# Optimization experiments

Hardware: AMD Instinct MI355X
Metric: run time of the kernel (lower is better)

## Reference

```python
import jax, jax.numpy as jnp
import numpy as np

N_NODES = 15
EMBED_DIM = 2048
F1 = 1024
F2 = 512
N_EDGES = 120


def gcn_conv(x, src, dst, W, b):
    # PyG GCNConv: h = D^{-1/2} (A + I) D^{-1/2} (x W) + b
    h = x @ W                                   # [N, F_out]
    n = h.shape[0]
    loops = jnp.arange(n)
    s = jnp.concatenate([src, loops])
    d = jnp.concatenate([dst, loops])
    deg = jax.ops.segment_sum(jnp.ones_like(d, dtype=h.dtype), d, num_segments=n)
    dinv = jax.lax.rsqrt(deg)                   # deg >= 1 due to self loops
    norm = dinv[s] * dinv[d]                    # [E+N]
    out = jax.ops.segment_sum(h[s] * norm[:, None], d, num_segments=n)
    return out + b


def attention_pool(x, attW):
    # SimGNN-style attention: global ctx = tanh(mean(x W)); scores = sigmoid(x @ ctx)
    ctx = jnp.tanh(jnp.mean(x @ attW, axis=0))  # [F2]
    scores = jax.nn.sigmoid(x @ ctx)            # [N]
    return x.T @ scores                         # [F2]


def setup_inputs() -> dict:
    key = jax.random.key(0)
    ks = jax.random.split(key, 16)
    d = {}
    d['features_1'] = jax.random.normal(ks[0], (N_NODES,), dtype=jnp.float32)
    d['edge_index_1'] = jax.random.randint(ks[1], (2, N_EDGES), 0, N_NODES, dtype=jnp.int32)
    d['target'] = jax.random.uniform(ks[2], (3,), dtype=jnp.float32)
    def lin(k, fi, fo):
        s = 1.0 / np.sqrt(fi)
        kw, kb = jax.random.split(k)
        return (jax.random.uniform(kw, (fi, fo), minval=-s, maxval=s, dtype=jnp.float32),
                jax.random.uniform(kb, (fo,), minval=-s, maxval=s, dtype=jnp.float32))
    d['W1'], d['b1'] = lin(ks[3], 15, 15 * 32)
    d['W2'], d['b2'] = lin(ks[4], 15 * 32, 15 * 128)
    d['W3'], d['b3'] = lin(ks[5], 15 * 128, 15 * EMBED_DIM)
    d['gW1'], d['gb1'] = lin(ks[6], EMBED_DIM, F1)
    d['gW2'], d['gb2'] = lin(ks[7], F1, F2)
    d['attW'] = jax.random.normal(ks[8], (F2, F2), dtype=jnp.float32) * (1.0 / np.sqrt(F2))
    d['fcW'], d['fcb'] = lin(ks[9], F2, 3)
    return d


def reference(features_1, edge_index_1, target, W1, b1, W2, b2, W3, b3,
              gW1, gb1, gW2, gb2, attW, fcW, fcb):
    # embed MLP: 15 -> 480 -> 1920 -> 15*embed_dim
    h = jax.nn.relu(features_1 @ W1 + b1)
    h = jax.nn.relu(h @ W2 + b2)
    h = (h @ W3 + b3).reshape(N_NODES, EMBED_DIM)
    src, dst = edge_index_1[0], edge_index_1[1]
    x = jax.nn.relu(gcn_conv(h, src, dst, gW1, gb1))
    x = gcn_conv(x, src, dst, gW2, gb2)
    rep = attention_pool(x, attW)               # [F2]
    logits = rep @ fcW + fcb                    # [3]
    cls = jnp.argmax(target)
    loss = -jax.nn.log_softmax(logits)[cls]
    predictions = jax.nn.softmax(logits)
    return loss, predictions
```

## Files before the change

### kernel.cpp

```cpp
#include <hip/hip_runtime.h>
#include <math.h>

#define NN 15
#define EMBED 2048
#define F1D 1024
#define F2D 512
#define NE 120
#define H1_DIM 480
#define H2_DIM 1920
#define H3_DIM 30720

#define OFF_A    0
#define OFF_H2   256
#define OFF_P3   2304
#define OFF_XG1  248064
#define OFF_P1   278784
#define OFF_XG2  524544
#define OFF_P2   539904
#define OFF_X2   662784
#define OFF_XBAR 670464
#define OFF_CTX  670976

__device__ inline void f4ma(float4& a, float s, const float4& w) {
    a.x += s * w.x; a.y += s * w.y; a.z += s * w.z; a.w += s * w.w;
}
__device__ inline void f4acc(float4& a, const float4& b) {
    a.x += b.x; a.y += b.y; a.z += b.z; a.w += b.w;
}

__global__ void k1_h2(const float* __restrict__ f, const float* __restrict__ W1,
                      const float* __restrict__ b1, const float* __restrict__ W2,
                      const float* __restrict__ b2, const int* __restrict__ edges,
                      float* __restrict__ ws) {
    int tid = threadIdx.x;
    if (blockIdx.x == 60) {
        __shared__ float dinv[NN];
        __shared__ float A[NN * NN];
        if (tid < NN) {
            int deg = 1;
            for (int i = 0; i < NE; ++i) deg += (edges[NE + i] == tid) ? 1 : 0;
            dinv[tid] = rsqrtf((float)deg);
        }
        __syncthreads();
        if (tid < NN * NN) {
            int r = tid / NN, c = tid % NN;
            A[tid] = (r == c) ? dinv[r] * dinv[r] : 0.0f;
        }
        __syncthreads();
        if (tid == 0) {
            for (int i = 0; i < NE; ++i) {
                int s = edges[i], d = edges[NE + i];
                A[d * NN + s] += dinv[s] * dinv[d];
            }
        }
        __syncthreads();
        if (tid < NN * NN) ws[OFF_A + tid] = A[tid];
        return;
    }
    __shared__ float h1[H1_DIM];
    __shared__ float4 red[32][8];
    float fr[NN];
#pragma unroll
    for (int k = 0; k < NN; ++k) fr[k] = f[k];
    for (int j = tid; j < H1_DIM; j += 256) {
        float acc = b1[j];
#pragma unroll
        for (int k = 0; k < NN; ++k) acc += fr[k] * W1[k * H1_DIM + j];
        h1[j] = fmaxf(acc, 0.0f);
    }
    __syncthreads();
    int jg = tid & 7, kc = tid >> 3;
    int j = blockIdx.x * 32 + jg * 4;
    float4 acc = make_float4(0.f, 0.f, 0.f, 0.f);
    for (int r = 0; r < 15; ++r) {
        int k = kc * 15 + r;
        float4 w = *(const float4*)(W2 + k * H2_DIM + j);
        f4ma(acc, h1[k], w);
    }
    red[kc][jg] = acc;
    __syncthreads();
    for (int s = 16; s >= 1; s >>= 1) {
        if (kc < s) f4acc(red[kc][jg], red[kc + s][jg]);
        __syncthreads();
    }
    if (kc == 0) {
        float4 b = *(const float4*)(b2 + j);
        float4 v = red[0][jg];
        v.x = fmaxf(v.x + b.x, 0.f); v.y = fmaxf(v.y + b.y, 0.f);
        v.z = fmaxf(v.z + b.z, 0.f); v.w = fmaxf(v.w + b.w, 0.f);
        *(float4*)(ws + OFF_H2 + j) = v;
    }
}

__global__ void k2_h3(const float* __restrict__ W3, float* __restrict__ ws) {
    __shared__ float h2l[240];
    __shared__ float cval[240];
    __shared__ int   coff[240];
    __shared__ int   wcnt[4];
    __shared__ int   nnz_s;
    __shared__ float4 red[128];
    int tid = threadIdx.x;
    int cb = blockIdx.x, kc = blockIdx.y;
    int kbase = kc * 240;
    if (tid < 240) h2l[tid] = ws[OFF_H2 + kbase + tid];
    int lane = tid & 63, wv = tid >> 6;
    bool act = (tid < 240) && (h2l[tid] != 0.0f);
    unsigned long long m = __ballot(act);
    if (lane == 0) wcnt[wv] = __popcll(m);
    __syncthreads();
    int off = 0;
#pragma unroll
    for (int w = 0; w < 4; ++w) off += (w < wv) ? wcnt[w] : 0;
    if (act) {
        int p = off + __popcll(m & ((1ull << lane) - 1ull));
        coff[p] = (kbase + tid) * H3_DIM;
        cval[p] = h2l[tid];
    }
    if (tid == 0) nnz_s = wcnt[0] + wcnt[1] + wcnt[2] + wcnt[3];
    __syncthreads();
    int nr = nnz_s;
    int f4i = tid & 127, rg = tid >> 7;
    int col = cb * 512 + f4i * 4;
    float4 acc = make_float4(0.f, 0.f, 0.f, 0.f);
#pragma unroll 4
    for (int r = rg; r < nr; r += 2) {
        const float4 w = *(const float4*)(W3 + (size_t)(coff[r] + col));
        f4ma(acc, cval[r], w);
    }
    __syncthreads();
    if (rg == 1) red[f4i] = acc;
    __syncthreads();
    if (rg == 0) {
        f4acc(acc, red[f4i]);
        *(float4*)(ws + OFF_P3 + (size_t)kc * H3_DIM + col) = acc;
    }
}

__global__ void k3_agg1(const float* __restrict__ b3, float* __restrict__ ws) {
    __shared__ float Al[NN * NN];
    __shared__ float S[NN][32];
    int tid = threadIdx.x;
    int c0 = blockIdx.x * 32;
    for (int i = tid; i < NN * NN; i += 256) Al[i] = ws[OFF_A + i];
    for (int q = tid; q < NN * 32; q += 256) {
        int m = q >> 5, c = q & 31;
        int j = m * EMBED + c0 + c;
        float s = b3[j];
#pragma unroll
        for (int p = 0; p < 8; ++p) s += ws[OFF_P3 + p * H3_DIM + j];
        S[m][c] = s;
    }
    __syncthreads();
    for (int q = tid; q < NN * 32; q += 256) {
        int n = q >> 5, c = q & 31;
        float x = 0.f;
#pragma unroll
        for (int m = 0; m < NN; ++m) x += Al[n * NN + m] * S[m][c];
        ws[OFF_XG1 + n * EMBED + c0 + c] = x;
    }
}

template<int IN, int OUT, int ECH>
__global__ void k_mmP(const float* __restrict__ X, const float* __restrict__ W,
                      float* __restrict__ P) {
    __shared__ float Xl[NN * ECH];
    __shared__ float4 red[8][32][NN];
    int tid = threadIdx.x;
    int e0 = blockIdx.y * ECH;
    for (int i = tid; i < NN * ECH; i += 256) {
        int n = i / ECH, e = i - n * ECH;
        Xl[i] = X[n * IN + e0 + e];
    }
    __syncthreads();
    int fg = tid & 31, kt = tid >> 5;
    int f = blockIdx.x * 128 + fg * 4;
    float4 acc[NN];
#pragma unroll
    for (int n = 0; n < NN; ++n) acc[n] = make_float4(0.f, 0.f, 0.f, 0.f);
    const int RPT = ECH / 8;
    for (int r = 0; r < RPT; ++r) {
        int e = kt * RPT + r;
        float4 w = *(const float4*)(W + (size_t)(e0 + e) * OUT + f);
#pragma unroll
        for (int n = 0; n < NN; ++n) f4ma(acc[n], Xl[n * ECH + e], w);
    }
    __syncthreads();
#pragma unroll
    for (int n = 0; n < NN; ++n) red[kt][fg][n] = acc[n];
    __syncthreads();
    for (int s = 4; s >= 1; s >>= 1) {
        if (kt < s) {
#pragma unroll
            for (int n = 0; n < NN; ++n) f4acc(red[kt][fg][n], red[kt + s][fg][n]);
        }
        __syncthreads();
    }
    if (kt == 0) {
#pragma unroll
        for (int n = 0; n < NN; ++n) {
            float4 v = red[0][fg][n];
            *(float4*)(P + (size_t)blockIdx.y * NN * OUT + n * OUT + f) = v;
        }
    }
}

__global__ void k5_fin1(const float* __restrict__ gb1, float* __restrict__ ws) {
    __shared__ float Al[NN * NN];
    __shared__ float S[NN][64];
    int tid = threadIdx.x;
    int f0 = blockIdx.x * 64;
    for (int i = tid; i < NN * NN; i += 256) Al[i] = ws[OFF_A + i];
    for (int q = tid; q < NN * 64; q += 256) {
        int n = q >> 6, c = q & 63;
        float s = gb1[f0 + c];
#pragma unroll
        for (int p = 0; p < 16; ++p) s += ws[OFF_P1 + p * (NN * F1D) + n * F1D + f0 + c];
        S[n][c] = fmaxf(s, 0.f);
    }
    __syncthreads();
    for (int q = tid; q < NN * 64; q += 256) {
        int n = q >> 6, c = q & 63;
        float x = 0.f;
#pragma unroll
        for (int m = 0; m < NN; ++m) x += Al[n * NN + m] * S[m][c];
        ws[OFF_XG2 + n * F1D + f0 + c] = x;
    }
}

__global__ void k7_fin2(const float* __restrict__ gb2, float* __restrict__ ws) {
    __shared__ float S[NN][64];
    int tid = threadIdx.x;
    int f0 = blockIdx.x * 64;
    for (int q = tid; q < NN * 64; q += 256) {
        int n = q >> 6, c = q & 63;
        float s = gb2[f0 + c];
#pragma unroll
        for (int p = 0; p < 16; ++p) s += ws[OFF_P2 + p * (NN * F2D) + n * F2D + f0 + c];
        S[n][c] = s;
        ws[OFF_X2 + n * F2D + f0 + c] = s;
    }
    __syncthreads();
    if (tid < 64) {
        float s = 0.f;
#pragma unroll
        for (int n = 0; n < NN; ++n) s += S[n][tid];
        ws[OFF_XBAR + f0 + tid] = s * (1.0f / 15.0f);
    }
}

__global__ void k8_ctx(const float* __restrict__ attW, float* __restrict__ ws) {
    __shared__ float xb[F2D];
    __shared__ float4 red[64][4];
    int tid = threadIdx.x;
    for (int e = tid; e < F2D; e += 256) xb[e] = ws[OFF_XBAR + e];
    __syncthreads();
    int fg = tid & 3, kt = tid >> 2;
    int f = blockIdx.x * 16 + fg * 4;
    float4 acc = make_float4(0.f, 0.f, 0.f, 0.f);
    for (int r = 0; r < 8; ++r) {
        int e = kt * 8 + r;
        float4 w = *(const float4*)(attW + e * F2D + f);
        f4ma(acc, xb[e], w);
    }
    red[kt][fg] = acc;
    __syncthreads();
    for (int s = 32; s >= 1; s >>= 1) {
        if (kt < s) f4acc(red[kt][fg], red[kt + s][fg]);
        __syncthreads();
    }
    if (kt == 0) {
        float4 v = red[0][fg];
        ws[OFF_CTX + f + 0] = tanhf(v.x);
        ws[OFF_CTX + f + 1] = tanhf(v.y);
        ws[OFF_CTX + f + 2] = tanhf(v.z);
        ws[OFF_CTX + f + 3] = tanhf(v.w);
    }
}

__global__ void k9_final(const float* __restrict__ fcW, const float* __restrict__ fcb,
                         const float* __restrict__ target, const float* __restrict__ ws,
                         float* __restrict__ out) {
    __shared__ float x2l[NN * F2D];
    __shared__ float ctxl[F2D];
    __shared__ float scores[16];
    __shared__ float rep[F2D];
    __shared__ float logits[3];
    int tid = threadIdx.x;
    for (int i = tid; i < NN * F2D; i += 256) x2l[i] = ws[OFF_X2 + i];
    for (int i = tid; i < F2D; i += 256) ctxl[i] = ws[OFF_CTX + i];
    __syncthreads();
    {
        int g = tid >> 4, l = tid & 15;
        if (g < NN) {
            float p = 0.f;
            for (int i = 0; i < 32; ++i) {
                int e = l + 16 * i;
                p += x2l[g * F2D + e] * ctxl[e];
            }
            p += __shfl_xor(p, 1); p += __shfl_xor(p, 2);
            p += __shfl_xor(p, 4); p += __shfl_xor(p, 8);
            if (l == 0) scores[g] = 1.0f / (1.0f + expf(-p));
        }
    }
    __syncthreads();
    for (int fi = tid; fi < F2D; fi += 256) {
        float v = 0.f;
#pragma unroll
        for (int n = 0; n < NN; ++n) v += x2l[n * F2D + fi] * scores[n];
        rep[fi] = v;
    }
    __syncthreads();
    if (tid < 192) {
        int j = tid >> 6, l = tid & 63;
        float p = 0.f;
        for (int i = 0; i < 8; ++i) {
            int e = l + 64 * i;
            p += rep[e] * fcW[e * 3 + j];
        }
        p += __shfl_xor(p, 1); p += __shfl_xor(p, 2); p += __shfl_xor(p, 4);
        p += __shfl_xor(p, 8); p += __shfl_xor(p, 16); p += __shfl_xor(p, 32);
        if (l == 0) logits[j] = p + fcb[j];
    }
    __syncthreads();
    if (tid == 0) {
        float t0 = target[0], t1 = target[1], t2 = target[2];
        int cls = 0; float best = t0;
        if (t1 > best) { best = t1; cls = 1; }
        if (t2 > best) { cls = 2; }
        float l0 = logits[0], l1 = logits[1], l2 = logits[2];
        float m = fmaxf(l0, fmaxf(l1, l2));
        float e0 = expf(l0 - m), e1 = expf(l1 - m), e2 = expf(l2 - m);
        float s = e0 + e1 + e2;
        float lc = (cls == 0) ? l0 : ((cls == 1) ? l1 : l2);
        out[0] = -(lc - m - logf(s));
        out[1] = e0 / s; out[2] = e1 / s; out[3] = e2 / s;
    }
}

extern "C" void kernel_launch(void* const* d_in, const int* in_sizes, int n_in,
                              void* d_out, int out_size, void* d_ws, size_t ws_size,
                              hipStream_t stream) {
    const float* f    = (const float*)d_in[0];
    const int*   ei   = (const int*)d_in[1];
    const float* tgt  = (const float*)d_in[2];
    const float* W1   = (const float*)d_in[3];
    const float* b1   = (const float*)d_in[4];
    const float* W2   = (const float*)d_in[5];
    const float* b2   = (const float*)d_in[6];
    const float* W3   = (const float*)d_in[7];
    const float* b3   = (const float*)d_in[8];
    const float* gW1  = (const float*)d_in[9];
    const float* gb1  = (const float*)d_in[10];
    const float* gW2  = (const float*)d_in[11];
    const float* gb2  = (const float*)d_in[12];
    const float* attW = (const float*)d_in[13];
    const float* fcW  = (const float*)d_in[14];
    const float* fcb  = (const float*)d_in[15];
    float* ws  = (float*)d_ws;
    float* out = (float*)d_out;

    k1_h2<<<dim3(61), dim3(256), 0, stream>>>(f, W1, b1, W2, b2, ei, ws);
    k2_h3<<<dim3(60, 8), dim3(256), 0, stream>>>(W3, ws);
    k3_agg1<<<dim3(64), dim3(256), 0, stream>>>(b3, ws);
    k_mmP<2048, 1024, 128><<<dim3(8, 16), dim3(256), 0, stream>>>(ws + OFF_XG1, gW1, ws + OFF_P1);
    k5_fin1<<<dim3(16), dim3(256), 0, stream>>>(gb1, ws);
    k_mmP<1024, 512, 64><<<dim3(4, 16), dim3(256), 0, stream>>>(ws + OFF_XG2, gW2, ws + OFF_P2);
    k7_fin2<<<dim3(8), dim3(256), 0, stream>>>(gb2, ws);
    k8_ctx<<<dim3(32), dim3(256), 0, stream>>>(attW, ws);
    k9_final<<<dim3(1), dim3(256), 0, stream>>>(fcW, fcb, tgt, ws, out);
}
```

Before: 383.4 us.

## Fuse GCN aggregation into matmul kernels and double the W3 split-K grid

Merges the bias, split-K reduction and adjacency aggregation stages into the following matmul kernels, so each block recomputes its own input slice in shared memory instead of writing and re-reading intermediate buffers. This cuts the launch count from nine to six. The W3 sparse GEMV split-K grid doubles from 8 to 16 K-chunks, which adds parallelism over the large weight stream. In exchange there is redundant work: each matmul block redoes the aggregation for its slice, and every ctx block re-reduces the whole P2 buffer.

```diff
diff --git a/kernel.cpp b/kernel.cpp
--- a/kernel.cpp
+++ b/kernel.cpp
@@ -13,13 +13,10 @@
 #define OFF_A    0
 #define OFF_H2   256
 #define OFF_P3   2304
-#define OFF_XG1  248064
-#define OFF_P1   278784
-#define OFF_XG2  524544
-#define OFF_P2   539904
-#define OFF_X2   662784
-#define OFF_XBAR 670464
-#define OFF_CTX  670976
+#define OFF_P1   493824
+#define OFF_P2   739584
+#define OFF_X2   862464
+#define OFF_CTX  870144
 
 __device__ inline void f4ma(float4& a, float s, const float4& w) {
     a.x += s * w.x; a.y += s * w.y; a.z += s * w.z; a.w += s * w.w;
@@ -93,32 +90,29 @@
 }
 
 __global__ void k2_h3(const float* __restrict__ W3, float* __restrict__ ws) {
-    __shared__ float h2l[240];
-    __shared__ float cval[240];
-    __shared__ int   coff[240];
+    __shared__ float h2l[120];
+    __shared__ float cval[120];
+    __shared__ int   coff[120];
     __shared__ int   wcnt[4];
-    __shared__ int   nnz_s;
     __shared__ float4 red[128];
     int tid = threadIdx.x;
     int cb = blockIdx.x, kc = blockIdx.y;
-    int kbase = kc * 240;
-    if (tid < 240) h2l[tid] = ws[OFF_H2 + kbase + tid];
+    int kbase = kc * 120;
+    float hv = 0.0f;
+    if (tid < 120) { hv = ws[OFF_H2 + kbase + tid]; h2l[tid] = hv; }
     int lane = tid & 63, wv = tid >> 6;
-    bool act = (tid < 240) && (h2l[tid] != 0.0f);
+    bool act = (tid < 120) && (hv != 0.0f);
     unsigned long long m = __ballot(act);
     if (lane == 0) wcnt[wv] = __popcll(m);
     __syncthreads();
-    int off = 0;
-#pragma unroll
-    for (int w = 0; w < 4; ++w) off += (w < wv) ? wcnt[w] : 0;
     if (act) {
+        int off = (wv == 1) ? wcnt[0] : 0;
         int p = off + __popcll(m & ((1ull << lane) - 1ull));
         coff[p] = (kbase + tid) * H3_DIM;
-        cval[p] = h2l[tid];
-    }
-    if (tid == 0) nnz_s = wcnt[0] + wcnt[1] + wcnt[2] + wcnt[3];
-    __syncthreads();
-    int nr = nnz_s;
+        cval[p] = hv;
+    }
+    __syncthreads();
+    int nr = wcnt[0] + wcnt[1];
     int f4i = tid & 127, rg = tid >> 7;
     int col = cb * 512 + f4i * 4;
     float4 acc = make_float4(0.f, 0.f, 0.f, 0.f);
@@ -136,40 +130,30 @@
     }
 }
 
-__global__ void k3_agg1(const float* __restrict__ b3, float* __restrict__ ws) {
+__global__ void k34_mm1(const float* __restrict__ b3, const float* __restrict__ gW1,
+                        float* __restrict__ ws) {
+    __shared__ float4 red[8][32][NN];
     __shared__ float Al[NN * NN];
-    __shared__ float S[NN][32];
-    int tid = threadIdx.x;
-    int c0 = blockIdx.x * 32;
+    __shared__ float Xl[NN * 128];
+    float* S = (float*)red;
+    int tid = threadIdx.x;
+    int e0 = blockIdx.y * 128;
     for (int i = tid; i < NN * NN; i += 256) Al[i] = ws[OFF_A + i];
-    for (int q = tid; q < NN * 32; q += 256) {
-        int m = q >> 5, c = q & 31;
-        int j = m * EMBED + c0 + c;
+    for (int q = tid; q < NN * 128; q += 256) {
+        int mm = q >> 7, c = q & 127;
+        int j = mm * EMBED + e0 + c;
         float s = b3[j];
 #pragma unroll
-        for (int p = 0; p < 8; ++p) s += ws[OFF_P3 + p * H3_DIM + j];
-        S[m][c] = s;
-    }
-    __syncthreads();
-    for (int q = tid; q < NN * 32; q += 256) {
-        int n = q >> 5, c = q & 31;
+        for (int p = 0; p < 16; ++p) s += ws[OFF_P3 + p * H3_DIM + j];
+        S[q] = s;
+    }
+    __syncthreads();
+    for (int q = tid; q < NN * 128; q += 256) {
+        int n = q >> 7, c = q & 127;
         float x = 0.f;
 #pragma unroll
-        for (int m = 0; m < NN; ++m) x += Al[n * NN + m] * S[m][c];
-        ws[OFF_XG1 + n * EMBED + c0 + c] = x;
-    }
-}
-
-template<int IN, int OUT, int ECH>
-__global__ void k_mmP(const float* __restrict__ X, const float* __restrict__ W,
-                      float* __restrict__ P) {
-    __shared__ float Xl[NN * ECH];
-    __shared__ float4 red[8][32][NN];
-    int tid = threadIdx.x;
-    int e0 = blockIdx.y * ECH;
-    for (int i = tid; i < NN * ECH; i += 256) {
-        int n = i / ECH, e = i - n * ECH;
-        Xl[i] = X[n * IN + e0 + e];
+        for (int mm = 0; mm < NN; ++mm) x += Al[n * NN + mm] * S[mm * 128 + c];
+        Xl[q] = x;
     }
     __syncthreads();
     int fg = tid & 31, kt = tid >> 5;
@@ -177,12 +161,11 @@
     float4 acc[NN];
 #pragma unroll
     for (int n = 0; n < NN; ++n) acc[n] = make_float4(0.f, 0.f, 0.f, 0.f);
-    const int RPT = ECH / 8;
-    for (int r = 0; r < RPT; ++r) {
-        int e = kt * RPT + r;
-        float4 w = *(const float4*)(W + (size_t)(e0 + e) * OUT + f);
-#pragma unroll
-        for (int n = 0; n < NN; ++n) f4ma(acc[n], Xl[n * ECH + e], w);
+    for (int r = 0; r < 16; ++r) {
+        int e = kt * 16 + r;
+        float4 w = *(const float4*)(gW1 + (size_t)(e0 + e) * F1D + f);
+#pragma unroll
+        for (int n = 0; n < NN; ++n) f4ma(acc[n], Xl[n * 128 + e], w);
     }
     __syncthreads();
 #pragma unroll
@@ -197,62 +180,85 @@
     }
     if (kt == 0) {
 #pragma unroll
-        for (int n = 0; n < NN; ++n) {
-            float4 v = red[0][fg][n];
-            *(float4*)(P + (size_t)blockIdx.y * NN * OUT + n * OUT + f) = v;
-        }
-    }
-}
-
-__global__ void k5_fin1(const float* __restrict__ gb1, float* __restrict__ ws) {
+        for (int n = 0; n < NN; ++n)
+            *(float4*)(ws + OFF_P1 + (size_t)blockIdx.y * NN * F1D + n * F1D + f) = red[0][fg][n];
+    }
+}
+
+__global__ void k56_mm2(const float* __restrict__ gb1, const float* __restrict__ gW2,
+                        float* __restrict__ ws) {
+    __shared__ float4 red[8][32][NN];
     __shared__ float Al[NN * NN];
-    __shared__ float S[NN][64];
-    int tid = threadIdx.x;
-    int f0 = blockIdx.x * 64;
+    __shared__ float Xl[NN * 64];
+    float* S = (float*)red;
+    int tid = threadIdx.x;
+    int e0 = blockIdx.y * 64;
     for (int i = tid; i < NN * NN; i += 256) Al[i] = ws[OFF_A + i];
     for (int q = tid; q < NN * 64; q += 256) {
-        int n = q >> 6, c = q & 63;
-        float s = gb1[f0 + c];
-#pragma unroll
-        for (int p = 0; p < 16; ++p) s += ws[OFF_P1 + p * (NN * F1D) + n * F1D + f0 + c];
-        S[n][c] = fmaxf(s, 0.f);
+        int mm = q >> 6, c = q & 63;
+        float s = gb1[e0 + c];
+#pragma unroll
+        for (int p = 0; p < 16; ++p) s += ws[OFF_P1 + p * (NN * F1D) + mm * F1D + e0 + c];
+        S[q] = fmaxf(s, 0.f);
     }
     __syncthreads();
     for (int q = tid; q < NN * 64; q += 256) {
         int n = q >> 6, c = q & 63;
         float x = 0.f;
 #pragma unroll
-        for (int m = 0; m < NN; ++m) x += Al[n * NN + m] * S[m][c];
-        ws[OFF_XG2 + n * F1D + f0 + c] = x;
-    }
-}
-
-__global__ void k7_fin2(const float* __restrict__ gb2, float* __restrict__ ws) {
-    __shared__ float S[NN][64];
-    int tid = threadIdx.x;
-    int f0 = blockIdx.x * 64;
-    for (int q = tid; q < NN * 64; q += 256) {
-        int n = q >> 6, c = q & 63;
-        float s = gb2[f0 + c];
-#pragma unroll
-        for (int p = 0; p < 16; ++p) s += ws[OFF_P2 + p * (NN * F2D) + n * F2D + f0 + c];
-        S[n][c] = s;
-        ws[OFF_X2 + n * F2D + f0 + c] = s;
-    }
-    __syncthreads();
-    if (tid < 64) {
-        float s = 0.f;
-#pragma unroll
-        for (int n = 0; n < NN; ++n) s += S[n][tid];
-        ws[OFF_XBAR + f0 + tid] = s * (1.0f / 15.0f);
-    }
-}
-
-__global__ void k8_ctx(const float* __restrict__ attW, float* __restrict__ ws) {
+        for (int mm = 0; mm < NN; ++mm) x += Al[n * NN + mm] * S[mm * 64 + c];
+        Xl[q] = x;
+    }
+    __syncthreads();
+    int fg = tid & 31, kt = tid >> 5;
+    int f = blockIdx.x * 128 + fg * 4;
+    float4 acc[NN];
+#pragma unroll
+    for (int n = 0; n < NN; ++n) acc[n] = make_float4(0.f, 0.f, 0.f, 0.f);
+    for (int r = 0; r < 8; ++r) {
+        int e = kt * 8 + r;
+        float4 w = *(const float4*)(gW2 + (size_t)(e0 + e) * F2D + f);
+#pragma unroll
+        for (int n = 0; n < NN; ++n) f4ma(acc[n], Xl[n * 64 + e], w);
+    }
+    __syncthreads();
+#pragma unroll
+    for (int n = 0; n < NN; ++n) red[kt][fg][n] = acc[n];
+    __syncthreads();
+    for (int s = 4; s >= 1; s >>= 1) {
+        if (kt < s) {
+#pragma unroll
+            for (int n = 0; n < NN; ++n) f4acc(red[kt][fg][n], red[kt + s][fg][n]);
+        }
+        __syncthreads();
+    }
+    if (kt == 0) {
+#pragma unroll
+        for (int n = 0; n < NN; ++n)
+            *(float4*)(ws + OFF_P2 + (size_t)blockIdx.y * NN * F2D + n * F2D + f) = red[0][fg][n];
+    }
+}
+
+__global__ void k78_ctx(const float* __restrict__ gb2, const float* __restrict__ attW,
+                        float* __restrict__ ws) {
+    __shared__ float S[NN * F2D];
     __shared__ float xb[F2D];
     __shared__ float4 red[64][4];
     int tid = threadIdx.x;
-    for (int e = tid; e < F2D; e += 256) xb[e] = ws[OFF_XBAR + e];
+    for (int q = tid; q < NN * F2D; q += 256) {
+        float s = gb2[q & 511];
+#pragma unroll
+        for (int p = 0; p < 16; ++p) s += ws[OFF_P2 + p * (NN * F2D) + q];
+        S[q] = s;
+        if (blockIdx.x == 0) ws[OFF_X2 + q] = s;
+    }
+    __syncthreads();
+    for (int c = tid; c < F2D; c += 256) {
+        float s = 0.f;
+#pragma unroll
+        for (int n = 0; n < NN; ++n) s += S[n * F2D + c];
+        xb[c] = s * (1.0f / 15.0f);
+    }
     __syncthreads();
     int fg = tid & 3, kt = tid >> 2;
     int f = blockIdx.x * 16 + fg * 4;
@@ -360,12 +366,9 @@
     float* out = (float*)d_out;
 
     k1_h2<<<dim3(61), dim3(256), 0, stream>>>(f, W1, b1, W2, b2, ei, ws);
-    k2_h3<<<dim3(60, 8), dim3(256), 0, stream>>>(W3, ws);
-    k3_agg1<<<dim3(64), dim3(256), 0, stream>>>(b3, ws);
-    k_mmP<2048, 1024, 128><<<dim3(8, 16), dim3(256), 0, stream>>>(ws + OFF_XG1, gW1, ws + OFF_P1);
-    k5_fin1<<<dim3(16), dim3(256), 0, stream>>>(gb1, ws);
-    k_mmP<1024, 512, 64><<<dim3(4, 16), dim3(256), 0, stream>>>(ws + OFF_XG2, gW2, ws + OFF_P2);
-    k7_fin2<<<dim3(8), dim3(256), 0, stream>>>(gb2, ws);
-    k8_ctx<<<dim3(32), dim3(256), 0, stream>>>(attW, ws);
+    k2_h3<<<dim3(60, 16), dim3(256), 0, stream>>>(W3, ws);
+    k34_mm1<<<dim3(8, 16), dim3(256), 0, stream>>>(b3, gW1, ws);
+    k56_mm2<<<dim3(4, 16), dim3(256), 0, stream>>>(gb1, gW2, ws);
+    k78_ctx<<<dim3(32), dim3(256), 0, stream>>>(gb2, attW, ws);
     k9_final<<<dim3(1), dim3(256), 0, stream>>>(fcW, fcb, tgt, ws, out);
 }
```

New measurement: 394.3 us. +2.9%, slower.
